# Kernel optimization log

Hardware: AMD Instinct MI355X
Metric: run time of the kernel (lower is better)

The kernel has to match this reference:

```python
import jax, jax.numpy as jnp
import numpy as np

B, T, V, D = 128, 128, 64, 32
Q, E, PLM = 5, 8, 768
D_STATIC, N_CLASS = 16, 2
ALPHA = 0.5


def _glorot(key, shape):
    lim = (6.0 / (shape[-2] + shape[-1])) ** 0.5
    return jax.random.uniform(key, shape, jnp.float32, -lim, lim)


def setup_inputs() -> dict:
    key = jax.random.key(0)
    ks = jax.random.split(key, 30)
    data = jax.random.normal(ks[0], (B, T, V), jnp.float32)
    mask = (jax.random.uniform(ks[1], (B, T, V)) < 0.3).astype(jnp.float32)
    P = jnp.concatenate([data, mask], axis=-1)  # [b, t, 2v]
    return {
        "P": P,
        "P_static": jax.random.normal(ks[2], (B, D_STATIC), jnp.float32),
        "P_avg_interval": jax.random.uniform(ks[3], (B, T, V)) * 10.0,
        "P_length": jax.random.randint(ks[4], (B, 1), T // 2, T + 1),
        "P_time": jax.random.uniform(ks[5], (B, T)),
        "P_var_plm_rep_tensor": jax.random.normal(ks[6], (V, PLM), jnp.float32),
        # Value_Encoder: Linear(1, D) + ReLU
        "w_val": _glorot(ks[7], (1, D))[0], "b_val": jnp.zeros((D,), jnp.float32),
        # Time_Encoder: periodic Linear(1, D-1), linear Linear(1, 1)
        "w_per": _glorot(ks[8], (1, D - 1))[0], "b_per": jnp.zeros((D - 1,), jnp.float32),
        "w_lin": _glorot(ks[9], (1, 1))[0], "b_lin": jnp.zeros((1,), jnp.float32),
        "emb1": jax.random.normal(ks[10], (V, D), jnp.float32),
        # prior_to_state MLP: PLM -> 2D -> Q
        "Ws1": _glorot(ks[11], (PLM, 2 * D)), "bs1": jnp.zeros((2 * D,), jnp.float32),
        "Ws2": _glorot(ks[12], (2 * D, Q)), "bs2": jnp.zeros((Q,), jnp.float32),
        # prior_to_graph MLP: PLM -> 2D -> E
        "Wg1": _glorot(ks[13], (PLM, 2 * D)), "bg1": jnp.zeros((2 * D,), jnp.float32),
        "Wg2": _glorot(ks[14], (2 * D, E)), "bg2": jnp.zeros((E,), jnp.float32),
        "rarity_W": jax.random.normal(ks[15], (V, V), jnp.float32),
        # hypernet gate params (nodes_num == Q): W [Q, 2D+1, D], b [Q, D]
        "Wu": _glorot(ks[16], (Q, 2 * D + 1, D)), "bu": _glorot(ks[17], (Q, D)),
        "Wr": _glorot(ks[18], (Q, 2 * D + 1, D)), "br": _glorot(ks[19], (Q, D)),
        "Wcand": _glorot(ks[20], (Q, 2 * D + 1, D)), "bcand": _glorot(ks[21], (Q, D)),
        # static embedding + classifier
        "W_se": _glorot(ks[22], (D_STATIC, V)), "b_se": jnp.zeros((V,), jnp.float32),
        "Wc1": _glorot(ks[23], (2 * V, 200)), "bc1": jnp.zeros((200,), jnp.float32),
        "Wc2": _glorot(ks[24], (200, N_CLASS)), "bc2": jnp.zeros((N_CLASS,), jnp.float32),
    }


def _forward(P, P_static, P_avg_interval, P_length, P_time, P_var_plm_rep_tensor,
             w_val, b_val, w_per, b_per, w_lin, b_lin, emb1,
             Ws1, bs1, Ws2, bs2, Wg1, bg1, Wg2, bg2, rarity_W,
             Wu, bu, Wr, br, Wcand, bcand, W_se, b_se, Wc1, bc1, Wc2, bc2):
    b, t, v2 = P.shape
    v = v2 // 2
    d = emb1.shape[1]
    data, mask = P[:, :, :v], P[:, :, v:]            # [b,t,v] each
    mk = mask[..., None]
    # embeddings: value + absolute time + node embedding, all masked
    value_emb = jax.nn.relu(data[..., None] * w_val + b_val) * mk          # [b,t,v,d]
    tt = P_time[:, :, None, None]                                          # [b,t,1,1]
    time_emb = jnp.concatenate([tt * w_lin + b_lin,
                                jnp.sin(tt * w_per + b_per)], -1) * mk     # [b,t,v,d]
    obs_emb = (value_emb + time_emb + emb1[None, None]) * mk               # [b,t,v,d]

    # PLM-prior hypernet vectors (identical across batch -> computed once, broadcast)
    var_vector = jax.nn.relu(P_var_plm_rep_tensor @ Ws1 + bs1) @ Ws2 + bs2  # [v,Q]
    gvec = jax.nn.relu(P_var_plm_rep_tensor @ Wg1 + bg1) @ Wg2 + bg2        # [v,E]
    gvec = gvec / jnp.maximum(jnp.linalg.norm(gvec, axis=-1, keepdims=True), 1e-12)
    adj = jax.nn.softmax(gvec @ gvec.T, axis=-1)                            # [v,v]

    var_total_obs = mask.sum(axis=1)                                        # [b,v]
    eye = jnp.eye(v, dtype=P.dtype)
    lengths = P_length[:, 0].astype(jnp.int32)                              # [b]

    def gate(inp, W, bb):
        # hypernet-generated per-node GRU gate: einsum('nd,dio->nio') + bmm, fused
        return (jnp.einsum('bvi,vq,qio->bvo', inp, var_vector, W)
                + jnp.einsum('vq,qo->vo', var_vector, bb))

    def step(carry, xs):
        h, out = carry
        cur_obs, m, cur_avg, s = xs
        rarity = ALPHA * jnp.tanh(cur_avg / (var_total_obs + 1.0))          # [b,v]
        rsm = -rarity_W * jnp.abs(rarity[:, :, None] - rarity[:, None, :])  # [b,v,v]
        amask = m[:, :, None] * m[:, None, :]   # rows of unobserved zeroed, observed cols = 1
        cur_adj = adj * (1.0 + rsm) * amask * (1.0 - eye) + eye             # [b,v,v]
        x = jnp.concatenate([cur_obs, rarity[..., None]], -1)               # [b,v,d+1]
        comb = jnp.einsum('bij,bjk->bik', cur_adj, jnp.concatenate([x, h], -1))
        r = jax.nn.sigmoid(gate(comb, Wr, br))
        u = jax.nn.sigmoid(gate(comb, Wu, bu))
        h_r = r * h  # original mutates h[nodes_ind] = r*h[nodes_ind] before candidate
        cand = jnp.tanh(gate(jnp.concatenate([x, h_r], -1), Wcand, bcand))
        h_new = (1.0 - u) * h_r + u * cand
        h = jnp.where((m > 0.5)[..., None], h_new, h)  # scatter only observed nodes
        out = jnp.where((s == lengths - 1)[:, None, None], h, out)
        return (h, out), None

    xs = (jnp.moveaxis(obs_emb, 1, 0), jnp.moveaxis(mask, 1, 0),
          jnp.moveaxis(P_avg_interval, 1, 0), jnp.arange(t, dtype=jnp.int32))
    h0 = jnp.zeros((b, v, d), P.dtype)
    (_, output), _ = jax.lax.scan(step, (h0, jnp.zeros_like(h0)), xs)

    static_emb = P_static @ W_se + b_se                                     # [b,v]
    feat = jnp.concatenate([output.sum(-1), static_emb], -1)                # [b,2v]
    return jax.nn.relu(feat @ Wc1 + bc1) @ Wc2 + bc2                        # [b,n_class]


def reference(P, P_static, P_avg_interval, P_length, P_time, P_var_plm_rep_tensor,
              w_val, b_val, w_per, b_per, w_lin, b_lin, emb1,
              Ws1, bs1, Ws2, bs2, Wg1, bg1, Wg2, bg2, rarity_W,
              Wu, bu, Wr, br, Wcand, bcand, W_se, b_se, Wc1, bc1, Wc2, bc2):
    return _forward(P, P_static, P_avg_interval, P_length, P_time, P_var_plm_rep_tensor,
                    w_val, b_val, w_per, b_per, w_lin, b_lin, emb1,
                    Ws1, bs1, Ws2, bs2, Wg1, bg1, Wg2, bg2, rarity_W,
                    Wu, bu, Wr, br, Wcand, bcand, W_se, b_se, Wc1, bc1, Wc2, bc2)
```

## Files before the change

kernel.cpp:

```cpp
#include <hip/hip_runtime.h>
#include <math.h>

#define BB 128
#define TT 128
#define VV 64
#define DD 32
#define NQ 5

typedef short bf16x8 __attribute__((ext_vector_type(8)));
typedef float f32x4 __attribute__((ext_vector_type(4)));

#define MFMA(a,b,c) __builtin_amdgcn_mfma_f32_16x16x32_bf16(a,b,c,0,0,0)

__device__ __forceinline__ float sigm(float x){ return 1.0f/(1.0f+__expf(-x)); }
__device__ __forceinline__ float tanhfast(float x){ return 2.0f/(1.0f+__expf(-2.0f*x)) - 1.0f; }
__device__ __forceinline__ unsigned short f2bf(float x){
  unsigned u = __float_as_uint(x);
  u += 0x7FFFu + ((u>>16)&1u);
  return (unsigned short)(u>>16);
}
__device__ __forceinline__ float bf2f(unsigned short h){
  return __uint_as_float(((unsigned)h)<<16);
}

union bfu { bf16x8 v; unsigned u[4]; unsigned short s[8]; };

__device__ __forceinline__ void split8(const float* x, bfu& H, bfu& L){
  #pragma unroll
  for (int i = 0; i < 8; ++i){
    const unsigned short hh = f2bf(x[i]);
    H.s[i] = hh;
    L.s[i] = f2bf(x[i] - bf2f(hh));
  }
}


__global__ __launch_bounds__(64)
void k_mlp(const float* __restrict__ Pplm,
           const float* __restrict__ Ws1, const float* __restrict__ bs1,
           const float* __restrict__ Ws2, const float* __restrict__ bs2,
           const float* __restrict__ Wg1, const float* __restrict__ bg1,
           const float* __restrict__ Wg2, const float* __restrict__ bg2,
           float* __restrict__ vv_ws, float* __restrict__ gn_ws)
{
  __shared__ float sH[64], sG[64], sgv[8];
  const int v = blockIdx.x, j = threadIdx.x;
  float a = bs1[j], g = bg1[j];
  for (int k = 0; k < 768; ++k){
    const float p = Pplm[v*768 + k];
    a = fmaf(p, Ws1[k*64 + j], a);
    g = fmaf(p, Wg1[k*64 + j], g);
  }
  sH[j] = fmaxf(a, 0.f);
  sG[j] = fmaxf(g, 0.f);
  __syncthreads();
  if (j < 5){
    float acc = bs2[j];
    for (int k = 0; k < 64; ++k) acc = fmaf(sH[k], Ws2[k*5 + j], acc);
    vv_ws[v*5 + j] = acc;
  }
  if (j < 8){
    float acc = bg2[j];
    for (int k = 0; k < 64; ++k) acc = fmaf(sG[k], Wg2[k*8 + j], acc);
    sgv[j] = acc;
  }
  __syncthreads();
  if (j == 0){
    float n = 0.f;
    for (int e = 0; e < 8; ++e) n += sgv[e]*sgv[e];
    n = fmaxf(sqrtf(n), 1e-12f);
    for (int e = 0; e < 8; ++e) gn_ws[v*8 + e] = sgv[e]/n;
  }
}

__global__ __launch_bounds__(64)
void k_adj(const float* __restrict__ gn_ws, float* __restrict__ adj_ws)
{
  const int v = blockIdx.x, j = threadIdx.x;
  float sc = 0.f;
  #pragma unroll
  for (int e = 0; e < 8; ++e) sc += gn_ws[v*8+e]*gn_ws[j*8+e];
  float mx = sc;
  for (int off = 32; off > 0; off >>= 1) mx = fmaxf(mx, __shfl_xor(mx, off));
  const float ex = __expf(sc - mx);
  float sm = ex;
  for (int off = 32; off > 0; off >>= 1) sm += __shfl_xor(sm, off);
  adj_ws[v*64 + j] = ex / sm;
}

__global__ __launch_bounds__(256)
void k_vto(const float* __restrict__ P, float* __restrict__ vto_ws)
{
  const int idx = blockIdx.x*256 + threadIdx.x;
  if (idx >= BB*VV) return;
  const int b = idx/VV, v = idx%VV;
  float s = 0.f;
  for (int t = 0; t < TT; ++t) s += P[((size_t)(b*TT+t))*128 + 64 + v];
  vto_ws[idx] = s;
}

__global__ __launch_bounds__(256)
void k_bpack(const float* __restrict__ Wr, const float* __restrict__ br,
             const float* __restrict__ Wu, const float* __restrict__ bu,
             const float* __restrict__ Wc, const float* __restrict__ bc,
             unsigned short* __restrict__ Bru, unsigned short* __restrict__ Bcn,
             float* __restrict__ sideRU, float* __restrict__ sideC)
{
  const int idx = blockIdx.x*256 + threadIdx.x;
  if (idx < 20480){
    const int f = idx >> 9, rem = idx & 511, l = rem >> 3, j = rem & 7;
    const int p = f & 1, kt = (f>>1)&1, e = f>>2;
    const int kp = kt*32 + (l>>4)*8 + j;
    const int k = (kp < 32) ? kp : kp + 1;
    const int o = p*16 + (l&15);
    const int q = (e < 5) ? e : e - 5;
    const float* W = (e < 5) ? Wr : Wu;
    Bru[idx] = f2bf(W[(q*65 + k)*32 + o]);
  } else if (idx < 30720){
    const int i2 = idx - 20480;
    const int f = i2 >> 9, rem = i2 & 511, l = rem >> 3, j = rem & 7;
    const int p = f & 1, kt = (f>>1)&1, e = f>>2;
    const int kp = kt*32 + (l>>4)*8 + j;
    const int k = (kp < 32) ? kp : kp + 1;
    const int o = p*16 + (l&15);
    Bcn[i2] = f2bf(Wc[(e*65 + k)*32 + o]);
  } else if (idx < 31360){
    const int i3 = idx - 30720;
    const int e = i3 >> 6, s = (i3 >> 5) & 1, o = i3 & 31;
    const int q = (e < 5) ? e : e - 5;
    float v;
    if (s == 0) v = (e < 5) ? Wr[(q*65 + 32)*32 + o] : Wu[(q*65 + 32)*32 + o];
    else        v = (e < 5) ? br[q*32 + o] : bu[q*32 + o];
    sideRU[i3] = v;
  } else if (idx < 31680){
    const int i4 = idx - 31360;
    const int e = i4 >> 6, s = (i4 >> 5) & 1, o = i4 & 31;
    sideC[i4] = s ? bc[e*32 + o] : Wc[(e*65 + 32)*32 + o];
  }
}


__global__ __launch_bounds__(256, 1)
void tedgn_main(const float* __restrict__ P, const float* __restrict__ Pstatic,
                const float* __restrict__ Pavg, const int* __restrict__ Plen,
                const float* __restrict__ Ptime,
                const float* __restrict__ w_val, const float* __restrict__ b_val,
                const float* __restrict__ w_per, const float* __restrict__ b_per,
                const float* __restrict__ w_lin, const float* __restrict__ b_lin,
                const float* __restrict__ emb1, const float* __restrict__ rarW,
                const float* __restrict__ Wse, const float* __restrict__ bse,
                const float* __restrict__ Wc1, const float* __restrict__ bc1,
                const float* __restrict__ Wc2, const float* __restrict__ bc2,
                const float* __restrict__ vv_ws, const float* __restrict__ adjb_ws,
                const float* __restrict__ vto_ws,
                const unsigned short* __restrict__ Bru_ws,
                const unsigned short* __restrict__ Bc_ws,
                const float* __restrict__ sideRU_ws, const float* __restrict__ sideC_ws,
                float* __restrict__ out)
{
  __shared__ __align__(16) unsigned short B0T[2][2][64][80];
  __shared__ __align__(16) unsigned short s_Wru[20480];
  __shared__ __align__(16) unsigned short s_Wc[10240];
  __shared__ __align__(16) float A1f[4][16][68];
  __shared__ __align__(16) float hrF[4][16][36];
  __shared__ __align__(16) float s_rar[2][64];
  __shared__ __align__(16) float s_m[2][64];
  __shared__ float s_sru[640], s_scd[320];
  __shared__ float s_outf[64][33];
  __shared__ float s_feat[128], s_hid[200];

  const int tid  = threadIdx.x;
  const int lane = tid & 63;
  const int wid  = tid >> 6;
  const int l15  = lane & 15;
  const int l16g = lane >> 4;
  const int kgo  = l16g * 8;
  const int R    = wid * 16;
  const int v_own = R + l15;
  const int b    = blockIdx.x;
  const int len  = Plen[b];

  for (int i = tid; i < 640; i += 256) s_sru[i] = sideRU_ws[i];
  for (int i = tid; i < 320; i += 256) s_scd[i] = sideC_ws[i];
  {
    const uint4* src1 = (const uint4*)Bru_ws;
    uint4* dst1 = (uint4*)s_Wru;
    for (int i = tid; i < 2560; i += 256) dst1[i] = src1[i];
    const uint4* src2 = (const uint4*)Bc_ws;
    uint4* dst2 = (uint4*)s_Wc;
    for (int i = tid; i < 1280; i += 256) dst2[i] = src2[i];
  }

  float adjb_r[2][8], rarW_r[2][8];
  #pragma unroll
  for (int kt = 0; kt < 2; ++kt)
    #pragma unroll
    for (int j = 0; j < 8; ++j){
      adjb_r[kt][j] = adjb_ws[v_own*64 + kt*32 + kgo + j];
      rarW_r[kt][j] = rarW   [v_own*64 + kt*32 + kgo + j];
    }
  float embr[8], wvr[8], bvr[8], wpr[8], bpr[8];
  #pragma unroll
  for (int j = 0; j < 8; ++j){
    const int d = kgo + j;
    embr[j] = emb1[v_own*DD + d];
    wvr[j]  = w_val[d];
    bvr[j]  = b_val[d];
    wpr[j]  = (d == 0) ? w_lin[0] : w_per[d-1];
    bpr[j]  = (d == 0) ? b_lin[0] : b_per[d-1];
  }
  float vvr[4][NQ];
  #pragma unroll
  for (int j = 0; j < 4; ++j)
    #pragma unroll
    for (int q = 0; q < NQ; ++q)
      vvr[j][q] = vv_ws[(R + l16g*4 + j)*NQ + q];
  const float vto_own = vto_ws[b*VV + v_own];

  float h[2][4]    = {{0.f,0.f,0.f,0.f},{0.f,0.f,0.f,0.f}};
  float outr[2][4] = {{0.f,0.f,0.f,0.f},{0.f,0.f,0.f,0.f}};
  bfu xfH, xfL;
  float rar_own, m_own;

  {
    const float pd = P[(size_t)(b*TT)*128 + v_own];
    const float pm = P[(size_t)(b*TT)*128 + 64 + v_own];
    const float pa = Pavg[(size_t)(b*TT)*VV + v_own];
    const float pt = Ptime[b*TT];
    const float rar_n = 0.5f * tanhfast(pa / (vto_own + 1.f));
    float xv[8];
    #pragma unroll
    for (int j = 0; j < 8; ++j){
      const int d = kgo + j;
      const float tearg = fmaf(pt, wpr[j], bpr[j]);
      const float te = (d == 0) ? tearg : __sinf(tearg);
      const float ve = fmaxf(fmaf(pd, wvr[j], bvr[j]), 0.f);
      xv[j] = (ve + te + embr[j]) * pm;
    }
    split8(xv, xfH, xfL);
    #pragma unroll
    for (int j = 0; j < 8; ++j){
      B0T[0][0][kgo + j][v_own] = xfH.s[j];
      B0T[0][1][kgo + j][v_own] = xfL.s[j];
    }
    *(uint2*)&B0T[0][0][32 + l15][R + l16g*4] = make_uint2(0u, 0u);
    *(uint2*)&B0T[0][1][32 + l15][R + l16g*4] = make_uint2(0u, 0u);
    *(uint2*)&B0T[0][0][48 + l15][R + l16g*4] = make_uint2(0u, 0u);
    *(uint2*)&B0T[0][1][48 + l15][R + l16g*4] = make_uint2(0u, 0u);
    if (l16g == 0){
      s_rar[0][v_own] = rar_n;
      s_m[0][v_own]   = pm;
    }
    rar_own = rar_n;
    m_own   = pm;
  }
  __syncthreads();

  #pragma clang loop unroll(disable)
  for (int t = 0; t < TT; ++t){
    const int cur = t & 1, nxt = cur ^ 1;

    float pd = 0.f, pm = 0.f, pa = 0.f, pt = 0.f;
    const bool more = (t + 1 < TT);
    if (more){
      pd = P[(size_t)(b*TT + t + 1)*128 + v_own];
      pm = P[(size_t)(b*TT + t + 1)*128 + 64 + v_own];
      pa = Pavg[(size_t)(b*TT + t + 1)*VV + v_own];
      pt = Ptime[b*TT + t + 1];
    }

    bfu aAh[2], aAl[2];
    float crar = 0.f;
    #pragma unroll
    for (int kt = 0; kt < 2; ++kt){
      const float4 r0 = *(const float4*)&s_rar[cur][kt*32 + kgo];
      const float4 r1 = *(const float4*)&s_rar[cur][kt*32 + kgo + 4];
      const float4 m0 = *(const float4*)&s_m[cur][kt*32 + kgo];
      const float4 m1 = *(const float4*)&s_m[cur][kt*32 + kgo + 4];
      const float rj[8] = {r0.x,r0.y,r0.z,r0.w,r1.x,r1.y,r1.z,r1.w};
      const float mj[8] = {m0.x,m0.y,m0.z,m0.w,m1.x,m1.y,m1.z,m1.w};
      float av[8];
      #pragma unroll
      for (int j = 0; j < 8; ++j){
        const int k = kt*32 + kgo + j;
        const float e1 = fmaf(-rarW_r[kt][j], fabsf(rar_own - rj[j]), 1.0f);
        const float a  = adjb_r[kt][j] * e1 * (m_own * mj[j]);
        av[j] = (k == v_own) ? 1.0f : a;
        crar = fmaf(av[j], rj[j], crar);
      }
      split8(av, aAh[kt], aAl[kt]);
    }
    crar += __shfl_xor(crar, 16);
    crar += __shfl_xor(crar, 32);
    if (l16g == 0) A1f[wid][l15][64] = crar;

    #pragma unroll
    for (int n = 0; n < 4; ++n){
      f32x4 acc = {0.f,0.f,0.f,0.f};
      #pragma unroll
      for (int kt = 0; kt < 2; ++kt){
        const bf16x8 bh = *(const bf16x8*)&B0T[cur][0][n*16 + l15][kt*32 + kgo];
        const bf16x8 bl = *(const bf16x8*)&B0T[cur][1][n*16 + l15][kt*32 + kgo];
        acc = MFMA(aAh[kt].v, bh, acc);
        acc = MFMA(aAl[kt].v, bh, acc);
        acc = MFMA(aAh[kt].v, bl, acc);
      }
      const int col = n*16 + l15;
      #pragma unroll
      for (int j = 0; j < 4; ++j) A1f[wid][l16g*4 + j][col] = acc[j];
    }
    __builtin_amdgcn_sched_barrier(0);

    bfu aH[2], aL[2];
    #pragma unroll
    for (int kt = 0; kt < 2; ++kt){
      float xv[8];
      *(float4*)&xv[0] = *(const float4*)&A1f[wid][l15][kt*32 + kgo];
      *(float4*)&xv[4] = *(const float4*)&A1f[wid][l15][kt*32 + kgo + 4];
      split8(xv, aH[kt], aL[kt]);
    }
    float a64f[4];
    #pragma unroll
    for (int j = 0; j < 4; ++j) a64f[j] = A1f[wid][l16g*4 + j][64];

    float hr[2][4];
    {
      f32x4 ag[5][2];
      #pragma unroll
      for (int e = 0; e < 5; ++e)
        #pragma unroll
        for (int p2 = 0; p2 < 2; ++p2){
          const int o = p2*16 + l15;
          const float w64 = s_sru[e*64 + o];
          const float bs  = s_sru[e*64 + 32 + o];
          #pragma unroll
          for (int j = 0; j < 4; ++j) ag[e][p2][j] = fmaf(a64f[j], w64, bs);
        }
      #pragma unroll
      for (int e = 0; e < 5; ++e)
        #pragma unroll
        for (int p2 = 0; p2 < 2; ++p2){
          const bf16x8 w0 = *(const bf16x8*)&s_Wru[(((e*2+0)*2+p2)*64 + lane)*8];
          const bf16x8 w1 = *(const bf16x8*)&s_Wru[(((e*2+1)*2+p2)*64 + lane)*8];
          ag[e][p2] = MFMA(aH[0].v, w0, ag[e][p2]);
          ag[e][p2] = MFMA(aL[0].v, w0, ag[e][p2]);
          ag[e][p2] = MFMA(aH[1].v, w1, ag[e][p2]);
          ag[e][p2] = MFMA(aL[1].v, w1, ag[e][p2]);
        }
      #pragma unroll
      for (int p2 = 0; p2 < 2; ++p2)
        #pragma unroll
        for (int j = 0; j < 4; ++j){
          const float pr = vvr[j][0]*ag[0][p2][j] + vvr[j][1]*ag[1][p2][j]
                         + vvr[j][2]*ag[2][p2][j] + vvr[j][3]*ag[3][p2][j]
                         + vvr[j][4]*ag[4][p2][j];
          hr[p2][j] = sigm(pr) * h[p2][j];
          hrF[wid][l16g*4 + j][p2*16 + l15] = hr[p2][j];
        }
    }
    __builtin_amdgcn_sched_barrier(0);

    float uu[2][4];
    {
      f32x4 ag[5][2];
      #pragma unroll
      for (int e = 0; e < 5; ++e)
        #pragma unroll
        for (int p2 = 0; p2 < 2; ++p2){
          const int o = p2*16 + l15;
          const float w64 = s_sru[(5 + e)*64 + o];
          const float bs  = s_sru[(5 + e)*64 + 32 + o];
          #pragma unroll
          for (int j = 0; j < 4; ++j) ag[e][p2][j] = fmaf(a64f[j], w64, bs);
        }
      #pragma unroll
      for (int e = 0; e < 5; ++e)
        #pragma unroll
        for (int p2 = 0; p2 < 2; ++p2){
          const bf16x8 w0 = *(const bf16x8*)&s_Wru[((((5+e)*2+0)*2+p2)*64 + lane)*8];
          const bf16x8 w1 = *(const bf16x8*)&s_Wru[((((5+e)*2+1)*2+p2)*64 + lane)*8];
          ag[e][p2] = MFMA(aH[0].v, w0, ag[e][p2]);
          ag[e][p2] = MFMA(aL[0].v, w0, ag[e][p2]);
          ag[e][p2] = MFMA(aH[1].v, w1, ag[e][p2]);
          ag[e][p2] = MFMA(aL[1].v, w1, ag[e][p2]);
        }
      #pragma unroll
      for (int p2 = 0; p2 < 2; ++p2)
        #pragma unroll
        for (int j = 0; j < 4; ++j){
          const float pu = vvr[j][0]*ag[0][p2][j] + vvr[j][1]*ag[1][p2][j]
                         + vvr[j][2]*ag[2][p2][j] + vvr[j][3]*ag[3][p2][j]
                         + vvr[j][4]*ag[4][p2][j];
          uu[p2][j] = sigm(pu);
        }
    }

    {
      bfu hH, hL;
      {
        float hv[8];
        *(float4*)&hv[0] = *(const float4*)&hrF[wid][l15][kgo];
        *(float4*)&hv[4] = *(const float4*)&hrF[wid][l15][kgo + 4];
        split8(hv, hH, hL);
      }
      float rar_cj[4], m_cj[4];
      #pragma unroll
      for (int j = 0; j < 4; ++j){
        rar_cj[j] = s_rar[cur][R + l16g*4 + j];
        m_cj[j]   = s_m[cur][R + l16g*4 + j];
      }
      f32x4 ag[5][2];
      #pragma unroll
      for (int e = 0; e < 5; ++e)
        #pragma unroll
        for (int p2 = 0; p2 < 2; ++p2){
          const int o = p2*16 + l15;
          const float w32 = s_scd[e*64 + o];
          const float bs  = s_scd[e*64 + 32 + o];
          #pragma unroll
          for (int j = 0; j < 4; ++j) ag[e][p2][j] = fmaf(rar_cj[j], w32, bs);
        }
      #pragma unroll
      for (int e = 0; e < 5; ++e)
        #pragma unroll
        for (int p2 = 0; p2 < 2; ++p2){
          const bf16x8 w0 = *(const bf16x8*)&s_Wc[(((e*2+0)*2+p2)*64 + lane)*8];
          const bf16x8 w1 = *(const bf16x8*)&s_Wc[(((e*2+1)*2+p2)*64 + lane)*8];
          ag[e][p2] = MFMA(xfH.v, w0, ag[e][p2]);
          ag[e][p2] = MFMA(xfL.v, w0, ag[e][p2]);
          ag[e][p2] = MFMA(hH.v,  w1, ag[e][p2]);
          ag[e][p2] = MFMA(hL.v,  w1, ag[e][p2]);
        }
      const bool snap = (t == len - 1);
      #pragma unroll
      for (int p2 = 0; p2 < 2; ++p2)
        #pragma unroll
        for (int j = 0; j < 4; ++j){
          const float pc = vvr[j][0]*ag[0][p2][j] + vvr[j][1]*ag[1][p2][j]
                         + vvr[j][2]*ag[2][p2][j] + vvr[j][3]*ag[3][p2][j]
                         + vvr[j][4]*ag[4][p2][j];
          const float cd = tanhfast(pc);
          const float hn = fmaf(uu[p2][j], cd - hr[p2][j], hr[p2][j]);
          const float hf = (m_cj[j] > 0.5f) ? hn : h[p2][j];
          h[p2][j] = hf;
          if (snap) outr[p2][j] = hf;
        }
    }

    {
      float h8[8] = {h[0][0],h[0][1],h[0][2],h[0][3],h[1][0],h[1][1],h[1][2],h[1][3]};
      bfu HH, HL;
      split8(h8, HH, HL);
      *(uint2*)&B0T[nxt][0][32 + l15][R + l16g*4] = make_uint2(HH.u[0], HH.u[1]);
      *(uint2*)&B0T[nxt][1][32 + l15][R + l16g*4] = make_uint2(HL.u[0], HL.u[1]);
      *(uint2*)&B0T[nxt][0][48 + l15][R + l16g*4] = make_uint2(HH.u[2], HH.u[3]);
      *(uint2*)&B0T[nxt][1][48 + l15][R + l16g*4] = make_uint2(HL.u[2], HL.u[3]);
    }

    if (more){
      const float rar_n = 0.5f * tanhfast(pa / (vto_own + 1.f));
      float xv[8];
      #pragma unroll
      for (int j = 0; j < 8; ++j){
        const int d = kgo + j;
        const float tearg = fmaf(pt, wpr[j], bpr[j]);
        const float te = (d == 0) ? tearg : __sinf(tearg);
        const float ve = fmaxf(fmaf(pd, wvr[j], bvr[j]), 0.f);
        xv[j] = (ve + te + embr[j]) * pm;
      }
      split8(xv, xfH, xfL);
      #pragma unroll
      for (int j = 0; j < 8; ++j){
        B0T[nxt][0][kgo + j][v_own] = xfH.s[j];
        B0T[nxt][1][kgo + j][v_own] = xfL.s[j];
      }
      if (l16g == 0){
        s_rar[nxt][v_own] = rar_n;
        s_m[nxt][v_own]   = pm;
      }
      rar_own = rar_n;
      m_own   = pm;
    }
    __syncthreads();
  }

  #pragma unroll
  for (int p2 = 0; p2 < 2; ++p2)
    #pragma unroll
    for (int j = 0; j < 4; ++j)
      s_outf[R + l16g*4 + j][p2*16 + l15] = outr[p2][j];
  __syncthreads();
  if (tid < VV){
    float s = 0.f;
    #pragma unroll
    for (int d = 0; d < DD; ++d) s += s_outf[tid][d];
    s_feat[tid] = s;
  } else if (tid < 2*VV){
    const int v = tid - VV;
    float se = bse[v];
    #pragma unroll
    for (int k = 0; k < 16; ++k) se = fmaf(Pstatic[b*16 + k], Wse[k*VV + v], se);
    s_feat[VV + v] = se;
  }
  __syncthreads();
  if (tid < 200){
    float a = bc1[tid];
    for (int k = 0; k < 128; ++k) a = fmaf(s_feat[k], Wc1[k*200 + tid], a);
    s_hid[tid] = fmaxf(a, 0.f);
  }
  __syncthreads();
  if (tid < 2){
    float a = bc2[tid];
    for (int k = 0; k < 200; ++k) a = fmaf(s_hid[k], Wc2[k*2 + tid], a);
    out[b*2 + tid] = a;
  }
}


extern "C" void kernel_launch(void* const* d_in, const int* in_sizes, int n_in,
                              void* d_out, int out_size, void* d_ws, size_t ws_size,
                              hipStream_t stream) {
  (void)in_sizes; (void)n_in; (void)out_size; (void)ws_size;
  const float* P       = (const float*)d_in[0];
  const float* Pstatic = (const float*)d_in[1];
  const float* Pavg    = (const float*)d_in[2];
  const int*   Plen    = (const int*)  d_in[3];
  const float* Ptime   = (const float*)d_in[4];
  const float* Pplm    = (const float*)d_in[5];
  const float* w_val   = (const float*)d_in[6];
  const float* b_val   = (const float*)d_in[7];
  const float* w_per   = (const float*)d_in[8];
  const float* b_per   = (const float*)d_in[9];
  const float* w_lin   = (const float*)d_in[10];
  const float* b_lin   = (const float*)d_in[11];
  const float* emb1    = (const float*)d_in[12];
  const float* Ws1     = (const float*)d_in[13];
  const float* bs1     = (const float*)d_in[14];
  const float* Ws2     = (const float*)d_in[15];
  const float* bs2     = (const float*)d_in[16];
  const float* Wg1     = (const float*)d_in[17];
  const float* bg1     = (const float*)d_in[18];
  const float* Wg2     = (const float*)d_in[19];
  const float* bg2     = (const float*)d_in[20];
  const float* rarW    = (const float*)d_in[21];
  const float* Wu      = (const float*)d_in[22];
  const float* bu      = (const float*)d_in[23];
  const float* Wr      = (const float*)d_in[24];
  const float* br      = (const float*)d_in[25];
  const float* Wcand   = (const float*)d_in[26];
  const float* bcand   = (const float*)d_in[27];
  const float* Wse     = (const float*)d_in[28];
  const float* bse     = (const float*)d_in[29];
  const float* Wc1     = (const float*)d_in[30];
  const float* bc1     = (const float*)d_in[31];
  const float* Wc2     = (const float*)d_in[32];
  const float* bc2     = (const float*)d_in[33];

  float* ws = (float*)d_ws;
  float*          vv_ws   = ws;
  float*          gn_ws   = ws + 320;
  float*          adjb_ws = ws + 832;
  float*          vto_ws  = ws + 4928;
  unsigned short* Bru_ws  = (unsigned short*)(ws + 13120);
  unsigned short* Bc_ws   = (unsigned short*)(ws + 23360);
  float*          sideRU_ws = ws + 28480;
  float*          sideC_ws  = ws + 29120;

  k_mlp  <<<64, 64, 0, stream>>>(Pplm, Ws1, bs1, Ws2, bs2, Wg1, bg1, Wg2, bg2, vv_ws, gn_ws);
  k_adj  <<<64, 64, 0, stream>>>(gn_ws, adjb_ws);
  k_vto  <<<(BB*VV + 255)/256, 256, 0, stream>>>(P, vto_ws);
  k_bpack<<<124, 256, 0, stream>>>(Wr, br, Wu, bu, Wcand, bcand, Bru_ws, Bc_ws, sideRU_ws, sideC_ws);

  tedgn_main<<<BB, 256, 0, stream>>>(P, Pstatic, Pavg, Plen, Ptime,
                                     w_val, b_val, w_per, b_per, w_lin, b_lin,
                                     emb1, rarW, Wse, bse, Wc1, bc1, Wc2, bc2,
                                     vv_ws, adjb_ws, vto_ws,
                                     Bru_ws, Bc_ws, sideRU_ws, sideC_ws,
                                     (float*)d_out);
}
```

Measured before the change: 660.7 us.

## Merge reset/update gate MFMA blocks, pack side weights, vectorize bf16 split

Fuses the reset and update gate hypernet MFMA blocks into one 10-edge accumulation so both can be scheduled together, and relaxes the scheduling barriers to sched_barrier(0x7F). It also interleaves the weight/bias side arrays so each lane fetches both values with a single float2 LDS load, uses the paired bf16 conversion intrinsic in the hi/lo split, and shrinks the B0T padding. The goal is more instruction-level overlap and fewer LDS instructions. In exchange the fused block keeps 80 accumulator registers live and the smaller padding may change LDS bank conflicts.

```diff
diff --git a/kernel.cpp b/kernel.cpp
--- a/kernel.cpp
+++ b/kernel.cpp
@@ -1,4 +1,5 @@
 #include <hip/hip_runtime.h>
+#include <hip/hip_bf16.h>
 #include <math.h>
 
 #define BB 128
@@ -11,6 +12,7 @@
 typedef float f32x4 __attribute__((ext_vector_type(4)));
 
 #define MFMA(a,b,c) __builtin_amdgcn_mfma_f32_16x16x32_bf16(a,b,c,0,0,0)
+#define SB_DS() __builtin_amdgcn_sched_barrier(0x7F)
 
 __device__ __forceinline__ float sigm(float x){ return 1.0f/(1.0f+__expf(-x)); }
 __device__ __forceinline__ float tanhfast(float x){ return 2.0f/(1.0f+__expf(-2.0f*x)) - 1.0f; }
@@ -27,10 +29,16 @@
 
 __device__ __forceinline__ void split8(const float* x, bfu& H, bfu& L){
   #pragma unroll
-  for (int i = 0; i < 8; ++i){
-    const unsigned short hh = f2bf(x[i]);
-    H.s[i] = hh;
-    L.s[i] = f2bf(x[i] - bf2f(hh));
+  for (int i = 0; i < 4; ++i){
+    const float a = x[2*i], c = x[2*i+1];
+    const __hip_bfloat162 hp = __float22bfloat162_rn(make_float2(a, c));
+    unsigned hu; __builtin_memcpy(&hu, &hp, 4);
+    H.u[i] = hu;
+    const float ah = __uint_as_float(hu << 16);
+    const float ch = __uint_as_float(hu & 0xFFFF0000u);
+    const __hip_bfloat162 lp = __float22bfloat162_rn(make_float2(a - ah, c - ch));
+    unsigned lu; __builtin_memcpy(&lu, &lp, 4);
+    L.u[i] = lu;
   }
 }
 
@@ -126,7 +134,7 @@
     Bcn[i2] = f2bf(Wc[(e*65 + k)*32 + o]);
   } else if (idx < 31360){
     const int i3 = idx - 30720;
-    const int e = i3 >> 6, s = (i3 >> 5) & 1, o = i3 & 31;
+    const int e = i3 >> 6, rem = i3 & 63, o = rem >> 1, s = rem & 1;
     const int q = (e < 5) ? e : e - 5;
     float v;
     if (s == 0) v = (e < 5) ? Wr[(q*65 + 32)*32 + o] : Wu[(q*65 + 32)*32 + o];
@@ -134,7 +142,7 @@
     sideRU[i3] = v;
   } else if (idx < 31680){
     const int i4 = idx - 31360;
-    const int e = i4 >> 6, s = (i4 >> 5) & 1, o = i4 & 31;
+    const int e = i4 >> 6, rem = i4 & 63, o = rem >> 1, s = rem & 1;
     sideC[i4] = s ? bc[e*32 + o] : Wc[(e*65 + 32)*32 + o];
   }
 }
@@ -158,7 +166,7 @@
                 const float* __restrict__ sideRU_ws, const float* __restrict__ sideC_ws,
                 float* __restrict__ out)
 {
-  __shared__ __align__(16) unsigned short B0T[2][2][64][80];
+  __shared__ __align__(16) unsigned short B0T[2][2][64][72];
   __shared__ __align__(16) unsigned short s_Wru[20480];
   __shared__ __align__(16) unsigned short s_Wc[10240];
   __shared__ __align__(16) float A1f[4][16][68];
@@ -309,7 +317,7 @@
       #pragma unroll
       for (int j = 0; j < 4; ++j) A1f[wid][l16g*4 + j][col] = acc[j];
     }
-    __builtin_amdgcn_sched_barrier(0);
+    SB_DS();
 
     bfu aH[2], aL[2];
     #pragma unroll
@@ -323,21 +331,19 @@
     #pragma unroll
     for (int j = 0; j < 4; ++j) a64f[j] = A1f[wid][l16g*4 + j][64];
 
-    float hr[2][4];
+    float hr[2][4], uu[2][4];
     {
-      f32x4 ag[5][2];
-      #pragma unroll
-      for (int e = 0; e < 5; ++e)
+      f32x4 ag[10][2];
+      #pragma unroll
+      for (int e = 0; e < 10; ++e)
         #pragma unroll
         for (int p2 = 0; p2 < 2; ++p2){
-          const int o = p2*16 + l15;
-          const float w64 = s_sru[e*64 + o];
-          const float bs  = s_sru[e*64 + 32 + o];
+          const float2 wb = *(const float2*)&s_sru[e*64 + (p2*16 + l15)*2];
           #pragma unroll
-          for (int j = 0; j < 4; ++j) ag[e][p2][j] = fmaf(a64f[j], w64, bs);
-        }
-      #pragma unroll
-      for (int e = 0; e < 5; ++e)
+          for (int j = 0; j < 4; ++j) ag[e][p2][j] = fmaf(a64f[j], wb.x, wb.y);
+        }
+      #pragma unroll
+      for (int e = 0; e < 10; ++e)
         #pragma unroll
         for (int p2 = 0; p2 < 2; ++p2){
           const bf16x8 w0 = *(const bf16x8*)&s_Wru[(((e*2+0)*2+p2)*64 + lane)*8];
@@ -357,43 +363,17 @@
           hr[p2][j] = sigm(pr) * h[p2][j];
           hrF[wid][l16g*4 + j][p2*16 + l15] = hr[p2][j];
         }
-    }
-    __builtin_amdgcn_sched_barrier(0);
-
-    float uu[2][4];
-    {
-      f32x4 ag[5][2];
-      #pragma unroll
-      for (int e = 0; e < 5; ++e)
-        #pragma unroll
-        for (int p2 = 0; p2 < 2; ++p2){
-          const int o = p2*16 + l15;
-          const float w64 = s_sru[(5 + e)*64 + o];
-          const float bs  = s_sru[(5 + e)*64 + 32 + o];
-          #pragma unroll
-          for (int j = 0; j < 4; ++j) ag[e][p2][j] = fmaf(a64f[j], w64, bs);
-        }
-      #pragma unroll
-      for (int e = 0; e < 5; ++e)
-        #pragma unroll
-        for (int p2 = 0; p2 < 2; ++p2){
-          const bf16x8 w0 = *(const bf16x8*)&s_Wru[((((5+e)*2+0)*2+p2)*64 + lane)*8];
-          const bf16x8 w1 = *(const bf16x8*)&s_Wru[((((5+e)*2+1)*2+p2)*64 + lane)*8];
-          ag[e][p2] = MFMA(aH[0].v, w0, ag[e][p2]);
-          ag[e][p2] = MFMA(aL[0].v, w0, ag[e][p2]);
-          ag[e][p2] = MFMA(aH[1].v, w1, ag[e][p2]);
-          ag[e][p2] = MFMA(aL[1].v, w1, ag[e][p2]);
-        }
       #pragma unroll
       for (int p2 = 0; p2 < 2; ++p2)
         #pragma unroll
         for (int j = 0; j < 4; ++j){
-          const float pu = vvr[j][0]*ag[0][p2][j] + vvr[j][1]*ag[1][p2][j]
-                         + vvr[j][2]*ag[2][p2][j] + vvr[j][3]*ag[3][p2][j]
-                         + vvr[j][4]*ag[4][p2][j];
+          const float pu = vvr[j][0]*ag[5][p2][j] + vvr[j][1]*ag[6][p2][j]
+                         + vvr[j][2]*ag[7][p2][j] + vvr[j][3]*ag[8][p2][j]
+                         + vvr[j][4]*ag[9][p2][j];
           uu[p2][j] = sigm(pu);
         }
     }
+    SB_DS();
 
     {
       bfu hH, hL;
@@ -414,11 +394,9 @@
       for (int e = 0; e < 5; ++e)
         #pragma unroll
         for (int p2 = 0; p2 < 2; ++p2){
-          const int o = p2*16 + l15;
-          const float w32 = s_scd[e*64 + o];
-          const float bs  = s_scd[e*64 + 32 + o];
+          const float2 wb = *(const float2*)&s_scd[e*64 + (p2*16 + l15)*2];
           #pragma unroll
-          for (int j = 0; j < 4; ++j) ag[e][p2][j] = fmaf(rar_cj[j], w32, bs);
+          for (int j = 0; j < 4; ++j) ag[e][p2][j] = fmaf(rar_cj[j], wb.x, wb.y);
         }
       #pragma unroll
       for (int e = 0; e < 5; ++e)
```

After: 623.4 us. 5.6% less time.
